# Performance work log

Measured on AMD Instinct MI355X. Metric: run time of the kernel, lower is better.

## Reference

```python
import jax, jax.numpy as jnp
import numpy as np

FFT_LEN = 512
HOP = 256
WIN_LEN = 1024


def setup_inputs() -> dict:
    key = jax.random.key(0)
    k1, k2 = jax.random.split(key)
    inputs = jax.random.normal(k1, (8, 514, 4000), dtype=jnp.float32)
    win = jax.random.uniform(k2, (WIN_LEN,), dtype=jnp.float32)
    return {"inputs": inputs, "win": win}


def reference(inputs, win):
    B, D, T = inputs.shape  # D == 514
    half = FFT_LEN // 2  # 256
    real = inputs[:, :half, :]            # [B,256,T]
    imag = inputs[:, half + 1:-1, :]      # [B,256,T]
    c = jax.lax.complex(real, imag)       # bins 0..255
    # conjugate-symmetric extension: bin 256 = 0, bins 257..511 = conj(bins 255..1)
    tail = jnp.conj(jnp.flip(c[:, 1:, :], axis=1))            # [B,255,T]
    zero = jnp.zeros_like(c[:, :1, :])
    spec = jnp.concatenate([c, zero, tail], axis=1)           # [B,512,T]
    # torch does fft over the freq axis and keeps the real part
    ifft_data = jnp.real(jnp.fft.fft(spec, axis=1)).astype(jnp.float32)  # [B,512,T]
    tmp = jnp.concatenate([ifft_data, ifft_data], axis=1)     # [B,1024,T]
    tmp = tmp * win[None, :, None] * 256.0
    # overlap-add via four shifted padded copies (faithful to the original)
    t1 = jnp.pad(tmp, ((0, 0), (0, 768), (0, 3)))
    t2 = jnp.pad(tmp, ((0, 0), (256, 512), (1, 2)))
    t3 = jnp.pad(tmp, ((0, 0), (512, 256), (2, 1)))
    t4 = jnp.pad(tmp, ((0, 0), (768, 0), (3, 0)))
    synbuf = t1 + t2 + t3 + t4                                # [B,1792,T+3]
    syn = synbuf[:, 768:1024, :-4]                            # [B,256,T-1]
    syn = jnp.flip(syn, axis=1)
    syn = jnp.transpose(syn, (0, 2, 1)).reshape(B, -1)        # [B,256*(T-1)]
    return syn
```

## Files before the change

kernel.cpp:

```cpp
#include <hip/hip_runtime.h>


typedef __attribute__((ext_vector_type(8))) short short8;
typedef __attribute__((ext_vector_type(8))) __bf16 bf16x8;
typedef __attribute__((ext_vector_type(4))) float floatx4;

__device__ inline short f2bf(float f) {
  unsigned u = __builtin_bit_cast(unsigned, f);
  u = (u + 0x7fffu + ((u >> 16) & 1u)) >> 16;
  return (short)(unsigned short)u;
}

#define PI_OVER_256 0.01227184630308513f

__global__ void build_m(short* __restrict__ M) {
  int idx = blockIdx.x * blockDim.x + threadIdx.x;
  int ntile = idx >> 10;
  int s = (idx >> 6) & 15;
  int lane = idx & 63;
  int n = ntile * 16 + (lane & 15);
  int kb = lane >> 4;
  short8 v;
#pragma unroll
  for (int e = 0; e < 8; e++) {
    int kap = s * 32 + kb * 8 + e;
    int gk = 2 * (kap & 255) + (kap >> 8);
    float val;
    if (gk == 0) {
      val = 1.0f;
    } else if (gk < 256) {
      int m = (n * gk) & 511;
      val = 2.0f * __cosf((float)m * PI_OVER_256);
    } else {
      int m = (n * (gk - 256)) & 511;
      val = 2.0f * __sinf((float)m * PI_OVER_256);
    }
    v[e] = f2bf(val);
  }
  ((short8*)M)[idx] = v;
}

__global__ __launch_bounds__(1024, 4) void gemm_ola(
    const float* __restrict__ in, const float* __restrict__ win,
    const short* __restrict__ M, float* __restrict__ out) {
  __shared__ short ldsX[64 * 512];

  const int tid = threadIdx.x;
  const int b = blockIdx.y;
  const int tile = blockIdx.x;
  const int c0 = 60 * tile - 4;

  {
    const int cbase = 4 * (tid & 15);
    const int kap0 = (tid >> 4) * 8;
    const int gc = c0 + cbase;
    const bool ok = (gc >= 0 && gc <= 3996);
    const float* src = in + (size_t)b * 2056000 + gc;
    floatx4 f[8];
    if (ok) {
#pragma unroll
      for (int j = 0; j < 8; j++) {
        int kap = kap0 + j;
        int gk = 2 * (kap & 255) + (kap >> 8);
        int row = (gk < 256) ? gk : gk + 1;
        f[j] = *(const floatx4*)(src + (size_t)row * 4000);
      }
    } else {
#pragma unroll
      for (int j = 0; j < 8; j++) f[j] = floatx4{0.f, 0.f, 0.f, 0.f};
    }
    const int g = kap0 >> 3;
#pragma unroll
    for (int cc = 0; cc < 4; cc++) {
      short8 v;
#pragma unroll
      for (int j = 0; j < 8; j++) v[j] = f2bf(f[j][cc]);
      const int col = cbase + cc;
      *(short8*)&ldsX[col * 512 + ((g ^ (col & 7)) << 3)] = v;
    }
  }
  __syncthreads();

  const int w = tid >> 6;
  const int lane = tid & 63;
  const int c = lane & 15;
  const int rg = lane >> 4;

  floatx4 accE[4] = {};
  floatx4 accO[4] = {};

  const short8* Mf = (const short8*)M;

  bf16x8 cb = __builtin_bit_cast(bf16x8, Mf[(w * 16 + 0) * 64 + lane]);

#pragma unroll
  for (int s = 0; s < 16; s++) {
    bf16x8 nb;
    if (s < 15) {
      nb = __builtin_bit_cast(bf16x8, Mf[(w * 16 + s + 1) * 64 + lane]);
    }
    const int g = 4 * s + rg;
    bf16x8 a[4];
#pragma unroll
    for (int q = 0; q < 4; q++) {
      const int col = 16 * q + c;
      a[q] = __builtin_bit_cast(
          bf16x8, *(const short8*)&ldsX[col * 512 + ((g ^ (c & 7)) << 3)]);
    }
    if (s < 8) {
#pragma unroll
      for (int q = 0; q < 4; q++)
        accE[q] = __builtin_amdgcn_mfma_f32_16x16x32_bf16(a[q], cb, accE[q], 0, 0, 0);
    } else {
#pragma unroll
      for (int q = 0; q < 4; q++)
        accO[q] = __builtin_amdgcn_mfma_f32_16x16x32_bf16(a[q], cb, accO[q], 0, 0, 0);
    }
    if (s < 15) cb = nb;
  }

  {
    const int j = 16 * w + c;
    const float wv0 = 256.0f * win[768 + j];
    const float wv1 = 256.0f * win[512 + j];
    const float wv2 = 256.0f * win[256 + j];
    const float wv3 = 256.0f * win[j];

    floatx4 Y[4], Yh[4];
#pragma unroll
    for (int q = 0; q < 4; q++) {
      Y[q] = accE[q] + accO[q];
      Yh[q] = accE[q] - accO[q];
    }

#pragma unroll
    for (int q = 0; q < 4; q++) {
      const int qm = (q > 0) ? q - 1 : 0;
      float yb[4], yhb[4];
#pragma unroll
      for (int p = 1; p < 4; p++) {
        float ia = __shfl(Y[q][p], lane - 16, 64);
        float pa = __shfl(Y[qm][p], lane + 48, 64);
        yb[p] = (rg > 0) ? ia : pa;
      }
#pragma unroll
      for (int p = 2; p < 4; p++) {
        float ia = __shfl(Yh[q][p], lane - 16, 64);
        float pa = __shfl(Yh[qm][p], lane + 48, 64);
        yhb[p] = (rg > 0) ? ia : pa;
      }
      floatx4 v;
#pragma unroll
      for (int p = 0; p < 4; p++) {
        float t1 = (p >= 1) ? Y[q][p - 1] : yb[3];
        float t2 = (p >= 2) ? Yh[q][p - 2] : yhb[p + 2];
        float t3 = (p >= 3) ? Y[q][p - 3] : yb[p + 1];
        v[p] = wv0 * Yh[q][p] + wv1 * t1 + wv2 * t2 + wv3 * t3;
      }
#pragma unroll
      for (int p = 0; p < 4; p++) {
        const int L = 16 * q + 4 * rg + p;
        const int t = c0 + L;
        if (L >= 4 && t <= 3998) {
          out[((size_t)b * 3999 + t) * 256 + (255 - j)] = v[p];
        }
      }
    }
  }
}

extern "C" void kernel_launch(void* const* d_in, const int* in_sizes, int n_in,
                              void* d_out, int out_size, void* d_ws, size_t ws_size,
                              hipStream_t stream) {
  const float* in = (const float*)d_in[0];
  const float* win = (const float*)d_in[1];
  float* out = (float*)d_out;
  short* M = (short*)d_ws;

  hipLaunchKernelGGL(build_m, dim3(64), dim3(256), 0, stream, M);
  hipLaunchKernelGGL(gemm_ola, dim3(67, 8), dim3(1024), 0, stream, in, win, M, out);
}
```

Baseline: 119.7 us.

## Pipeline global input staging with MFMA compute in four K-chunks

Splits the input staging into four K-chunks of 128. Each next chunk's global loads are issued before the MFMA work on the current chunk and written to LDS afterwards, with a barrier per chunk. The load mapping also changes from float4 loads over 4 columns to scalar loads with one column per thread. This aims to hide global-load latency behind compute, but it adds three barriers and uses narrower, less vectorized loads. The column bound check changes from 3996 to 3999 because of the per-column granularity.

```diff
diff --git a/kernel.cpp b/kernel.cpp
--- a/kernel.cpp
+++ b/kernel.cpp
@@ -50,74 +50,85 @@
   const int tile = blockIdx.x;
   const int c0 = 60 * tile - 4;
 
-  {
-    const int cbase = 4 * (tid & 15);
-    const int kap0 = (tid >> 4) * 8;
-    const int gc = c0 + cbase;
-    const bool ok = (gc >= 0 && gc <= 3996);
-    const float* src = in + (size_t)b * 2056000 + gc;
-    floatx4 f[8];
-    if (ok) {
-#pragma unroll
-      for (int j = 0; j < 8; j++) {
-        int kap = kap0 + j;
-        int gk = 2 * (kap & 255) + (kap >> 8);
-        int row = (gk < 256) ? gk : gk + 1;
-        f[j] = *(const floatx4*)(src + (size_t)row * 4000);
-      }
-    } else {
-#pragma unroll
-      for (int j = 0; j < 8; j++) f[j] = floatx4{0.f, 0.f, 0.f, 0.f};
-    }
-    const int g = kap0 >> 3;
-#pragma unroll
-    for (int cc = 0; cc < 4; cc++) {
-      short8 v;
-#pragma unroll
-      for (int j = 0; j < 8; j++) v[j] = f2bf(f[j][cc]);
-      const int col = cbase + cc;
-      *(short8*)&ldsX[col * 512 + ((g ^ (col & 7)) << 3)] = v;
-    }
-  }
-  __syncthreads();
+  const int scol = tid & 63;
+  const int skg = tid >> 6;
+  const int sgc = c0 + scol;
+  const bool sok = (sgc >= 0 && sgc <= 3999);
+  const float* src = in + (size_t)b * 2056000 + sgc;
 
   const int w = tid >> 6;
   const int lane = tid & 63;
   const int c = lane & 15;
   const int rg = lane >> 4;
+  const short8* Mf = (const short8*)M;
+
+  float fst[8];
+
+#define ISSUE_LOADS(CH)                                              \
+  {                                                                  \
+    _Pragma("unroll") for (int e = 0; e < 8; e++) {                  \
+      const int kap = (CH) * 128 + skg * 8 + e;                      \
+      const int gk = 2 * (kap & 255) + (kap >> 8);                   \
+      const int row = (gk < 256) ? gk : gk + 1;                      \
+      fst[e] = sok ? src[(size_t)row * 4000] : 0.f;                  \
+    }                                                                \
+  }
+
+#define WRITE_CHUNK(CH)                                              \
+  {                                                                  \
+    short8 v;                                                        \
+    _Pragma("unroll") for (int e = 0; e < 8; e++) v[e] = f2bf(fst[e]); \
+    const int g = (CH) * 16 + skg;                                   \
+    *(short8*)&ldsX[scol * 512 + ((g ^ (scol & 7)) << 3)] = v;       \
+  }
+
+  ISSUE_LOADS(0);
+  WRITE_CHUNK(0);
+  __syncthreads();
 
   floatx4 accE[4] = {};
   floatx4 accO[4] = {};
 
-  const short8* Mf = (const short8*)M;
-
   bf16x8 cb = __builtin_bit_cast(bf16x8, Mf[(w * 16 + 0) * 64 + lane]);
 
 #pragma unroll
-  for (int s = 0; s < 16; s++) {
-    bf16x8 nb;
-    if (s < 15) {
-      nb = __builtin_bit_cast(bf16x8, Mf[(w * 16 + s + 1) * 64 + lane]);
+  for (int ch = 0; ch < 4; ch++) {
+    if (ch < 3) ISSUE_LOADS(ch + 1);
+
+#pragma unroll
+    for (int si = 0; si < 4; si++) {
+      const int s = 4 * ch + si;
+      bf16x8 nb;
+      if (s < 15) {
+        nb = __builtin_bit_cast(bf16x8, Mf[(w * 16 + s + 1) * 64 + lane]);
+      }
+      const int g = 4 * s + rg;
+      bf16x8 a[4];
+#pragma unroll
+      for (int q = 0; q < 4; q++) {
+        const int col = 16 * q + c;
+        a[q] = __builtin_bit_cast(
+            bf16x8, *(const short8*)&ldsX[col * 512 + ((g ^ (c & 7)) << 3)]);
+      }
+      if (s < 8) {
+#pragma unroll
+        for (int q = 0; q < 4; q++)
+          accE[q] = __builtin_amdgcn_mfma_f32_16x16x32_bf16(a[q], cb, accE[q], 0, 0, 0);
+      } else {
+#pragma unroll
+        for (int q = 0; q < 4; q++)
+          accO[q] = __builtin_amdgcn_mfma_f32_16x16x32_bf16(a[q], cb, accO[q], 0, 0, 0);
+      }
+      if (s < 15) cb = nb;
     }
-    const int g = 4 * s + rg;
-    bf16x8 a[4];
-#pragma unroll
-    for (int q = 0; q < 4; q++) {
-      const int col = 16 * q + c;
-      a[q] = __builtin_bit_cast(
-          bf16x8, *(const short8*)&ldsX[col * 512 + ((g ^ (c & 7)) << 3)]);
+
+    if (ch < 3) {
+      WRITE_CHUNK(ch + 1);
+      __syncthreads();
     }
-    if (s < 8) {
-#pragma unroll
-      for (int q = 0; q < 4; q++)
-        accE[q] = __builtin_amdgcn_mfma_f32_16x16x32_bf16(a[q], cb, accE[q], 0, 0, 0);
-    } else {
-#pragma unroll
-      for (int q = 0; q < 4; q++)
-        accO[q] = __builtin_amdgcn_mfma_f32_16x16x32_bf16(a[q], cb, accO[q], 0, 0, 0);
-    }
-    if (s < 15) cb = nb;
   }
+#undef ISSUE_LOADS
+#undef WRITE_CHUNK
 
   {
     const int j = 16 * w + c;
```

Measured after the change: 117.8 us. No clear change (-1.5%).

## Shrink blocks to 4 waves, each computing four output tiles

Applied to the files above, without the earlier changes.

The workgroup drops from 16 waves to 4, and each wave now computes four 16-column output tiles instead of one. Each A fragment read from LDS is reused across four MFMAs, and each thread loads four times as much input during the staging phase. This cuts LDS reads per MFMA and wave scheduling overhead. In exchange it raises register pressure (32 accumulators plus 4 B fragments) and lowers wave-level parallelism per workgroup, which could hurt latency hiding given only 536 blocks.

```diff
diff --git a/kernel.cpp b/kernel.cpp
--- a/kernel.cpp
+++ b/kernel.cpp
@@ -40,7 +40,7 @@
   ((short8*)M)[idx] = v;
 }
 
-__global__ __launch_bounds__(1024, 4) void gemm_ola(
+__global__ __launch_bounds__(256, 1) void gemm_ola(
     const float* __restrict__ in, const float* __restrict__ win,
     const short* __restrict__ M, float* __restrict__ out) {
   __shared__ short ldsX[64 * 512];
@@ -52,31 +52,35 @@
 
   {
     const int cbase = 4 * (tid & 15);
-    const int kap0 = (tid >> 4) * 8;
+    const int kbase = (tid >> 4) * 32;
     const int gc = c0 + cbase;
     const bool ok = (gc >= 0 && gc <= 3996);
     const float* src = in + (size_t)b * 2056000 + gc;
-    floatx4 f[8];
-    if (ok) {
-#pragma unroll
-      for (int j = 0; j < 8; j++) {
-        int kap = kap0 + j;
-        int gk = 2 * (kap & 255) + (kap >> 8);
-        int row = (gk < 256) ? gk : gk + 1;
-        f[j] = *(const floatx4*)(src + (size_t)row * 4000);
-      }
-    } else {
-#pragma unroll
-      for (int j = 0; j < 8; j++) f[j] = floatx4{0.f, 0.f, 0.f, 0.f};
-    }
-    const int g = kap0 >> 3;
-#pragma unroll
-    for (int cc = 0; cc < 4; cc++) {
-      short8 v;
-#pragma unroll
-      for (int j = 0; j < 8; j++) v[j] = f2bf(f[j][cc]);
-      const int col = cbase + cc;
-      *(short8*)&ldsX[col * 512 + ((g ^ (col & 7)) << 3)] = v;
+#pragma unroll
+    for (int bt = 0; bt < 4; bt++) {
+      const int kap0 = kbase + 8 * bt;
+      floatx4 f[8];
+      if (ok) {
+#pragma unroll
+        for (int j = 0; j < 8; j++) {
+          int kap = kap0 + j;
+          int gk = 2 * (kap & 255) + (kap >> 8);
+          int row = (gk < 256) ? gk : gk + 1;
+          f[j] = *(const floatx4*)(src + (size_t)row * 4000);
+        }
+      } else {
+#pragma unroll
+        for (int j = 0; j < 8; j++) f[j] = floatx4{0.f, 0.f, 0.f, 0.f};
+      }
+      const int g = kap0 >> 3;
+#pragma unroll
+      for (int cc = 0; cc < 4; cc++) {
+        short8 v;
+#pragma unroll
+        for (int j = 0; j < 8; j++) v[j] = f2bf(f[j][cc]);
+        const int col = cbase + cc;
+        *(short8*)&ldsX[col * 512 + ((g ^ (col & 7)) << 3)] = v;
+      }
     }
   }
   __syncthreads();
@@ -86,18 +90,24 @@
   const int c = lane & 15;
   const int rg = lane >> 4;
 
-  floatx4 accE[4] = {};
-  floatx4 accO[4] = {};
+  floatx4 accE[4][4] = {};
+  floatx4 accO[4][4] = {};
 
   const short8* Mf = (const short8*)M;
 
-  bf16x8 cb = __builtin_bit_cast(bf16x8, Mf[(w * 16 + 0) * 64 + lane]);
+  bf16x8 cb[4];
+#pragma unroll
+  for (int jt = 0; jt < 4; jt++)
+    cb[jt] = __builtin_bit_cast(bf16x8, Mf[((4 * w + jt) * 16 + 0) * 64 + lane]);
 
 #pragma unroll
   for (int s = 0; s < 16; s++) {
-    bf16x8 nb;
+    bf16x8 nb[4];
     if (s < 15) {
-      nb = __builtin_bit_cast(bf16x8, Mf[(w * 16 + s + 1) * 64 + lane]);
+#pragma unroll
+      for (int jt = 0; jt < 4; jt++)
+        nb[jt] = __builtin_bit_cast(
+            bf16x8, Mf[((4 * w + jt) * 16 + s + 1) * 64 + lane]);
     }
     const int g = 4 * s + rg;
     bf16x8 a[4];
@@ -110,17 +120,27 @@
     if (s < 8) {
 #pragma unroll
       for (int q = 0; q < 4; q++)
-        accE[q] = __builtin_amdgcn_mfma_f32_16x16x32_bf16(a[q], cb, accE[q], 0, 0, 0);
+#pragma unroll
+        for (int jt = 0; jt < 4; jt++)
+          accE[q][jt] = __builtin_amdgcn_mfma_f32_16x16x32_bf16(
+              a[q], cb[jt], accE[q][jt], 0, 0, 0);
     } else {
 #pragma unroll
       for (int q = 0; q < 4; q++)
-        accO[q] = __builtin_amdgcn_mfma_f32_16x16x32_bf16(a[q], cb, accO[q], 0, 0, 0);
-    }
-    if (s < 15) cb = nb;
-  }
-
-  {
-    const int j = 16 * w + c;
+#pragma unroll
+        for (int jt = 0; jt < 4; jt++)
+          accO[q][jt] = __builtin_amdgcn_mfma_f32_16x16x32_bf16(
+              a[q], cb[jt], accO[q][jt], 0, 0, 0);
+    }
+    if (s < 15) {
+#pragma unroll
+      for (int jt = 0; jt < 4; jt++) cb[jt] = nb[jt];
+    }
+  }
+
+#pragma unroll
+  for (int jt = 0; jt < 4; jt++) {
+    const int j = 16 * (4 * w + jt) + c;
     const float wv0 = 256.0f * win[768 + j];
     const float wv1 = 256.0f * win[512 + j];
     const float wv2 = 256.0f * win[256 + j];
@@ -129,8 +149,8 @@
     floatx4 Y[4], Yh[4];
 #pragma unroll
     for (int q = 0; q < 4; q++) {
-      Y[q] = accE[q] + accO[q];
-      Yh[q] = accE[q] - accO[q];
+      Y[q] = accE[q][jt] + accO[q][jt];
+      Yh[q] = accE[q][jt] - accO[q][jt];
     }
 
 #pragma unroll
@@ -178,5 +198,5 @@
   short* M = (short*)d_ws;
 
   hipLaunchKernelGGL(build_m, dim3(64), dim3(256), 0, stream, M);
-  hipLaunchKernelGGL(gemm_ola, dim3(67, 8), dim3(1024), 0, stream, in, win, M, out);
-}
+  hipLaunchKernelGGL(gemm_ola, dim3(67, 8), dim3(256), 0, stream, in, win, M, out);
+}
```

Measured after the change: 126.3 us. +5.6%, slower.
